# Kernel tuning notes

Hardware: AMD Instinct MI355X
Metric: run time of the kernel (lower is better)

## Reference

```python
import jax, jax.numpy as jnp
import numpy as np

DIM = 2048
HEADS = 16
DIM_HEAD = 128
FF_INNER = DIM * 4
SCALE_BASE = 512
EPS = 1e-5


def setup_inputs() -> dict:
    key = jax.random.key(0)
    k1, k2, k3, k4 = jax.random.split(key, 4)
    fused_out = HEADS * DIM_HEAD + DIM_HEAD + DIM_HEAD + 2 * FF_INNER  # 18688
    x = jax.random.normal(k1, (2, 2048, DIM), dtype=jnp.float32)
    gamma = jnp.ones((DIM,), dtype=jnp.float32)
    W_fused = jax.random.normal(k2, (DIM, fused_out), dtype=jnp.float32) * 0.02
    W_attn_out = jax.random.normal(k3, (HEADS * DIM_HEAD, DIM), dtype=jnp.float32) * 0.02
    W_ff_out = jax.random.normal(k4, (FF_INNER, DIM), dtype=jnp.float32) * 0.02
    return {"x": x, "gamma": gamma, "W_fused": W_fused, "W_attn_out": W_attn_out, "W_ff_out": W_ff_out}


def _rotate_half(t):
    t1, t2 = jnp.split(t, 2, axis=-1)
    return jnp.concatenate((-t2, t1), axis=-1)


def _rotary(n, dtype):
    # RotaryEmbedding with use_xpos=True, scale_base=512
    half = DIM_HEAD // 2
    inv_freq = 1.0 / (10000.0 ** (jnp.arange(0, DIM_HEAD, 2, dtype=dtype) / DIM_HEAD))
    t = jnp.arange(n, dtype=dtype)
    freqs = jnp.einsum('i,j->ij', t, inv_freq)          # [n, half]
    freqs = jnp.concatenate((freqs, freqs), axis=-1)    # [n, dh]
    scale_vec = (jnp.arange(0, DIM_HEAD, 2, dtype=dtype) + 0.4 * DIM_HEAD) / (1.4 * DIM_HEAD)
    power = (t - n // 2) / SCALE_BASE
    scale = scale_vec[None, :] ** power[:, None]        # [n, half]
    scale = jnp.concatenate((scale, scale), axis=-1)    # [n, dh]
    return freqs, scale


def _apply_rope(pos, t, scale):
    return t * jnp.cos(pos) * scale + _rotate_half(t) * jnp.sin(pos) * scale


def reference(x, gamma, W_fused, W_attn_out, W_ff_out):
    b, n, d = x.shape
    # LayerNorm (beta fixed at zero)
    mu = jnp.mean(x, axis=-1, keepdims=True)
    var = jnp.var(x, axis=-1, keepdims=True)
    xn = (x - mu) * jax.lax.rsqrt(var + EPS) * gamma

    proj = xn @ W_fused
    attn_inner = HEADS * DIM_HEAD
    q = proj[..., :attn_inner]
    k = proj[..., attn_inner:attn_inner + DIM_HEAD]
    v = proj[..., attn_inner + DIM_HEAD:attn_inner + 2 * DIM_HEAD]
    ff = proj[..., attn_inner + 2 * DIM_HEAD:]

    q = q.reshape(b, n, HEADS, DIM_HEAD).transpose(0, 2, 1, 3)  # b h n d

    pos, scale = _rotary(n, x.dtype)
    q = _apply_rope(pos, q, scale)            # broadcasts [n,dh] over b,h
    k = _apply_rope(pos, k, 1.0 / scale)      # k is [b, n, dh]

    # multi-query attention, causal
    sim = jnp.einsum('bhid,bjd->bhij', q, k) * (DIM_HEAD ** -0.5)
    causal_mask = jnp.triu(jnp.ones((n, n), dtype=bool), 1)
    sim = jnp.where(causal_mask, jnp.finfo(sim.dtype).min, sim)
    attn = jax.nn.softmax(sim, axis=-1)
    out = jnp.einsum('bhij,bjd->bhid', attn, v)
    out = out.transpose(0, 2, 1, 3).reshape(b, n, attn_inner)
    attn_out = out @ W_attn_out

    # SwiGLU: chunk -> silu(gate) * x
    ff_x, ff_gate = jnp.split(ff, 2, axis=-1)
    ff_out = (jax.nn.silu(ff_gate) * ff_x) @ W_ff_out

    return attn_out + ff_out
```

## Files before the change

### kernel.cpp

```cpp
#include <hip/hip_runtime.h>

typedef __attribute__((ext_vector_type(8))) short short8;
typedef __attribute__((ext_vector_type(4))) float floatx4;
typedef __attribute__((ext_vector_type(8))) unsigned short ushort8;
typedef __attribute__((ext_vector_type(2))) unsigned int uint2v;

#define FOUT 18688
#define FFI  8192
#define CATW 10240

__device__ __forceinline__ float b2f(unsigned short u){
  union { unsigned int i; float f; } v; v.i = ((unsigned int)u) << 16; return v.f;
}
__device__ __forceinline__ unsigned short f2b(float f){
  union { float f; unsigned int i; } v; v.f = f;
  unsigned int r = v.i + 0x7FFFu + ((v.i >> 16) & 1u);
  return (unsigned short)(r >> 16);
}
__device__ __forceinline__ void gld_lds16(const void* g, void* l){
  __builtin_amdgcn_global_load_lds((const __attribute__((address_space(1))) void*)g,
                                   (__attribute__((address_space(3))) void*)l, 16, 0, 0);
}

__global__ __launch_bounds__(256) void ln_kernel(const float* __restrict__ x,
                                                 const float* __restrict__ gamma,
                                                 unsigned short* __restrict__ xn){
  int row = blockIdx.x;
  const float* xr = x + (size_t)row * 2048;
  int tid = threadIdx.x;
  float v[8]; float s = 0.f, s2 = 0.f;
#pragma unroll
  for(int i=0;i<8;i++){ float t = xr[tid + i*256]; v[i]=t; s+=t; s2+=t*t; }
#pragma unroll
  for(int off=32; off>=1; off>>=1){ s += __shfl_down(s, off, 64); s2 += __shfl_down(s2, off, 64); }
  __shared__ float red[8];
  int wv = tid>>6, ln_ = tid&63;
  if(ln_==0){ red[wv] = s; red[wv+4] = s2; }
  __syncthreads();
  s  = red[0]+red[1]+red[2]+red[3];
  s2 = red[4]+red[5]+red[6]+red[7];
  float mu  = s * (1.f/2048.f);
  float var = s2 * (1.f/2048.f) - mu*mu;
  float rstd = rsqrtf(var + 1e-5f);
#pragma unroll
  for(int i=0;i<8;i++){
    float o = (v[i]-mu)*rstd*gamma[tid + i*256];
    xn[(size_t)row*2048 + tid + i*256] = f2b(o);
  }
}

__global__ void tcast_kernel(const float* __restrict__ W, unsigned short* __restrict__ Wt,
                             int R, int C, int S, int O){
  __shared__ float t[32][33];
  int bx = blockIdx.x*32, by = blockIdx.y*32;
  int tx = threadIdx.x, ty = threadIdx.y;
#pragma unroll
  for(int i=0;i<4;i++) t[ty+i*8][tx] = W[(size_t)(by+ty+i*8)*C + bx+tx];
  __syncthreads();
#pragma unroll
  for(int i=0;i<4;i++) Wt[(size_t)(bx+ty+i*8)*S + O + by+tx] = f2b(t[tx][ty+i*8]);
}

__global__ void vtrans_kernel(const unsigned short* __restrict__ proj, unsigned short* __restrict__ vt){
  __shared__ unsigned short t[32][33];
  int b = blockIdx.z;
  int n0 = blockIdx.x*32, d0 = blockIdx.y*32;
  int tx = threadIdx.x, ty = threadIdx.y;
#pragma unroll
  for(int i=0;i<4;i++) t[ty+i*8][tx] = proj[(size_t)(b*2048 + n0+ty+i*8)*FOUT + 2176 + d0+tx];
  __syncthreads();
#pragma unroll
  for(int i=0;i<4;i++) vt[((size_t)b*128 + d0+ty+i*8)*2048 + n0+tx] = t[tx][ty+i*8];
}

__global__ __launch_bounds__(256) void rope_tab_kernel(floatx4* __restrict__ tab){
  int idx = blockIdx.x*256 + threadIdx.x;
  int i = idx >> 6, j = idx & 63;
  float fj = (float)j, fi = (float)i;
  float p = fi * powf(10000.f, -fj*(1.f/64.f));
  float c = cosf(p), s = sinf(p);
  float sv = (2.f*fj + 51.2f) * (1.f/179.2f);
  float pw = (fi - 1024.f) * (1.f/512.f);
  float sc = powf(sv, pw);
  const float att = 0.08838834764831843f;
  floatx4 o; o[0]=c*sc*att; o[1]=s*sc*att; o[2]=c/sc; o[3]=s/sc;
  tab[idx] = o;
}

__global__ __launch_bounds__(256) void rope_kernel(unsigned short* __restrict__ proj,
                                                   const floatx4* __restrict__ tab){
  int row = blockIdx.x;
  int i = row & 2047;
  unsigned short* pr = proj + (size_t)row*FOUT;
  for(int item = threadIdx.x; item < 17*64; item += 256){
    int slot = item >> 6;
    int j = item & 63;
    floatx4 t = tab[i*64 + j];
    float cs = (slot==16) ? t[2] : t[0];
    float ss = (slot==16) ? t[3] : t[1];
    int colbase = (slot<16) ? slot*128 : 2048;
    float x1 = b2f(pr[colbase+j]);
    float x2 = b2f(pr[colbase+j+64]);
    pr[colbase+j]    = f2b(x1*cs - x2*ss);
    pr[colbase+j+64] = f2b(x2*cs + x1*ss);
  }
}

#define SCHED0() __builtin_amdgcn_sched_barrier(0)
#define BARR()   do{ SCHED0(); __builtin_amdgcn_s_barrier(); SCHED0(); }while(0)

template<int MODE>
__global__ __launch_bounds__(512, 2) void gemm8p_kernel(const unsigned short* __restrict__ A,
                                                        const unsigned short* __restrict__ Bt,
                                                        unsigned short* __restrict__ Cb,
                                                        float* __restrict__ Cf,
                                                        int N, int K, int NT, int ntn,
                                                        size_t zstride){
  __shared__ unsigned short lds[65536];
  const int tid = threadIdx.x;
  const int wave = tid>>6, lane = tid&63;
  const int l15 = lane&15, l4 = lane>>4;
  const int wr = wave>>2, wc = wave&3;
  int id = blockIdx.x;
  int cpx = (int)gridDim.x >> 3;
  int swz = (id & 7)*cpx + (id >> 3);
  int tm = swz / ntn, tn = swz - tm*ntn;
  int kbase = (int)blockIdx.z * (NT*64);
  const unsigned short* Ab = A  + (size_t)tm*256*K + kbase;
  const unsigned short* Bb = Bt + (size_t)tn*256*K + kbase;
  if(MODE==1) Cf += (size_t)blockIdx.z * zstride;

  const int r0 = tid>>3;
  const int colc = ((tid&7) ^ (r0&7))*8;
  const int dstw = wave*512;

#define STAGE(t_, h_, isB_) do{ \
    const unsigned short* g_ = (isB_) ? Bb : Ab; \
    int db_ = (((t_)&1)<<15) + ((isB_)<<14) + ((h_)<<13) + dstw; \
    gld_lds16(g_ + (size_t)((h_)*128 + r0)*K + (t_)*64 + colc, &lds[db_]); \
    gld_lds16(g_ + (size_t)((h_)*128 + r0 + 64)*K + (t_)*64 + colc, &lds[db_ + 4096]); \
  }while(0)

  const int sw8 = l15&7;
  const int fo0 = ((l4    )^sw8)*8;
  const int fo1 = ((l4 + 4)^sw8)*8;
  const int albase = (wr*128 + l15)*64;
  const int blbase = 16384 + (wc*64 + l15)*64;

#define RD_A0(buf_, mf_, kk_) a0_[(mf_)*2+(kk_)] = *(const short8*)&lds[(buf_) + albase + (mf_)*1024 + ((kk_)?fo1:fo0)]
#define RD_A1(buf_, mf_, kk_) a1_[(mf_)*2+(kk_)] = *(const short8*)&lds[(buf_) + albase + 4096 + (mf_)*1024 + ((kk_)?fo1:fo0)]
#define RD_B(buf_, nf_, kk_)  b_[(nf_)*2+(kk_)]  = *(const short8*)&lds[(buf_) + blbase + (nf_)*1024 + ((kk_)?fo1:fo0)]
#define MFMA_Q(aarr_, mo_, no_) do{ \
  _Pragma("unroll") for(int kk=0; kk<2; kk++) \
  _Pragma("unroll") for(int mf=0; mf<4; mf++) \
  _Pragma("unroll") for(int nf=0; nf<2; nf++) \
    acc[(mo_)*4+mf][(no_)*2+nf] = __builtin_amdgcn_mfma_f32_16x16x32_bf16( \
      b_[((no_)*2+nf)*2+kk], aarr_[mf*2+kk], acc[(mo_)*4+mf][(no_)*2+nf], 0,0,0); \
}while(0)

  floatx4 acc[8][4];
#pragma unroll
  for(int i=0;i<8;i++)
#pragma unroll
    for(int j=0;j<4;j++) acc[i][j] = (floatx4)0.f;

  short8 a0_[8], a1_[8], b_[8];

  STAGE(0,0,0); STAGE(0,1,0); STAGE(0,0,1); STAGE(0,1,1);
  STAGE(1,0,1); STAGE(1,1,1); STAGE(1,0,0);
  asm volatile("s_waitcnt vmcnt(6)" ::: "memory");
  SCHED0();
  BARR();
#pragma unroll
  for(int mf=0; mf<4; mf++){ RD_A0(0,mf,0); RD_A0(0,mf,1); }
#pragma unroll
  for(int nf=0; nf<2; nf++){ RD_B(0,nf,0); RD_B(0,nf,1); }
  SCHED0();

  for(int t=0; t<NT; ++t){
    const int bufo = (t&1)<<15;
    const int nbuf = bufo ^ 32768;
    if(t+1 < NT) STAGE(t+1,1,0);
    BARR();
    RD_B(bufo,2,0); RD_B(bufo,2,1); RD_B(bufo,3,0); RD_B(bufo,3,1);
    asm volatile("s_waitcnt lgkmcnt(4)" ::: "memory");
    SCHED0();
    __builtin_amdgcn_s_setprio(1);
    MFMA_Q(a0_,0,0);
    __builtin_amdgcn_s_setprio(0);
    BARR();
    if(t+2 < NT) STAGE(t+2,0,1);
    BARR();
#pragma unroll
    for(int mf=0; mf<4; mf++){ RD_A1(bufo,mf,0); RD_A1(bufo,mf,1); }
    asm volatile("s_waitcnt lgkmcnt(8)" ::: "memory");
    SCHED0();
    __builtin_amdgcn_s_setprio(1);
    MFMA_Q(a0_,0,1);
    __builtin_amdgcn_s_setprio(0);
    BARR();
    if(t+2 < NT){
      STAGE(t+2,1,1);
      asm volatile("s_waitcnt vmcnt(8)" ::: "memory");
    } else if(t+1 < NT){
      asm volatile("s_waitcnt vmcnt(4)" ::: "memory");
    }
    SCHED0();
    BARR();
    asm volatile("s_waitcnt lgkmcnt(0)" ::: "memory");
    SCHED0();
    __builtin_amdgcn_s_setprio(1);
    MFMA_Q(a1_,1,0);
    __builtin_amdgcn_s_setprio(0);
    SCHED0();
    if(t+1 < NT){ RD_B(nbuf,0,0); RD_B(nbuf,0,1); RD_B(nbuf,1,0); RD_B(nbuf,1,1); }
    BARR();
    if(t+2 < NT){
      STAGE(t+2,0,0);
      asm volatile("s_waitcnt vmcnt(6)" ::: "memory");
    } else if(t+1 < NT){
      asm volatile("s_waitcnt vmcnt(0)" ::: "memory");
    }
    SCHED0();
    BARR();
    if(t+1 < NT){
#pragma unroll
      for(int mf=0; mf<4; mf++){ RD_A0(nbuf,mf,0); RD_A0(nbuf,mf,1); }
    }
    SCHED0();
    __builtin_amdgcn_s_setprio(1);
    MFMA_Q(a1_,1,1);
    __builtin_amdgcn_s_setprio(0);
    BARR();
  }

  const size_t crow0 = (size_t)tm*256 + wr*128 + l15;
  const size_t ccol0 = (size_t)tn*256 + wc*64 + l4*4;
#pragma unroll
  for(int mi=0; mi<8; mi++){
    size_t row = crow0 + (mi>>2)*64 + (mi&3)*16;
#pragma unroll
    for(int nj=0; nj<4; nj++){
      size_t col = ccol0 + nj*16;
      floatx4 v = acc[mi][nj];
      if(MODE==0){
        uint2v u;
        u[0] = (unsigned int)f2b(v[0]) | ((unsigned int)f2b(v[1])<<16);
        u[1] = (unsigned int)f2b(v[2]) | ((unsigned int)f2b(v[3])<<16);
        *(uint2v*)&Cb[row*N + col] = u;
      } else {
        *(floatx4*)&Cf[row*N + col] = v;
      }
    }
  }
}

__global__ __launch_bounds__(256) void add2_kernel(const float* __restrict__ p0,
                                                   const float* __restrict__ p1,
                                                   float* __restrict__ o, int n4){
  for(int i = blockIdx.x*256 + threadIdx.x; i < n4; i += gridDim.x*256){
    floatx4 a = ((const floatx4*)p0)[i];
    floatx4 b = ((const floatx4*)p1)[i];
    ((floatx4*)o)[i] = a + b;
  }
}

__global__ __launch_bounds__(256) void attn_kernel(const unsigned short* __restrict__ proj,
                                                   const unsigned short* __restrict__ vt,
                                                   unsigned short* __restrict__ ao){
  __shared__ unsigned short lK[64*128];
  __shared__ unsigned short lV[128*64];
  __shared__ unsigned short lP[4*16*64];
  int qt = blockIdx.x, hh = blockIdx.y, b = blockIdx.z;
  int tid = threadIdx.x, wave = tid>>6, lane = tid&63;
  int l15 = lane&15, l4 = lane>>4;
  int q0 = qt*64;
  int qrow = q0 + wave*16 + l15;
  const unsigned short* qp = proj + (size_t)(b*2048 + qrow)*FOUT + hh*128 + l4*8;
  short8 qf[4];
#pragma unroll
  for(int ds=0; ds<4; ds++) qf[ds] = *(const short8*)(qp + ds*32);
  floatx4 po[8];
#pragma unroll
  for(int dt=0; dt<8; dt++) po[dt] = (floatx4)0.f;
  float mrun[4] = {-1e30f,-1e30f,-1e30f,-1e30f};
  float lrun[4] = {0.f,0.f,0.f,0.f};
  unsigned short* lPw = lP + wave*1024;
  const unsigned short* kb = proj + (size_t)(b*2048)*FOUT + 2048;
  const unsigned short* vb = vt + (size_t)b*128*2048;

  for(int kv=0; kv<=qt; kv++){
    int kv0 = kv*64;
#pragma unroll
    for(int it=0; it<4; it++){
      int f = it*256 + tid;
      int r = f>>4, pc = f&15;
      int gc = pc ^ (r&7);
      gld_lds16(kb + (size_t)(kv0 + r)*FOUT + gc*8, &lK[(it*256 + wave*64)*8]);
    }
#pragma unroll
    for(int it=0; it<4; it++){
      int f = it*256 + tid;
      int d = f>>3, pc = f&7;
      int gc = pc ^ (d&7);
      gld_lds16(vb + (size_t)d*2048 + kv0 + gc*8, &lV[(it*256 + wave*64)*8]);
    }
    __syncthreads();
    floatx4 sa[4];
#pragma unroll
    for(int jt=0;jt<4;jt++) sa[jt] = (floatx4)0.f;
#pragma unroll
    for(int jt=0;jt<4;jt++){
      int krow = jt*16 + l15;
#pragma unroll
      for(int ds=0; ds<4; ds++){
        int pc = (l4 + ds*4) ^ (krow&7);
        short8 kf = *(const short8*)&lK[krow*128 + pc*8];
        sa[jt] = __builtin_amdgcn_mfma_f32_16x16x32_bf16(qf[ds], kf, sa[jt], 0,0,0);
      }
    }
    float pv[4][4];
    bool diag = (kv == qt);
#pragma unroll
    for(int jt=0;jt<4;jt++){
#pragma unroll
      for(int r=0;r<4;r++){
        float s = sa[jt][r];
        if(diag && (kv0 + jt*16 + l15 > q0 + wave*16 + l4*4 + r)) s = -1e30f;
        pv[jt][r] = s;
      }
    }
    float mnew[4], corr[4];
#pragma unroll
    for(int r=0;r<4;r++){
      float mx = fmaxf(fmaxf(pv[0][r],pv[1][r]),fmaxf(pv[2][r],pv[3][r]));
      mx = fmaxf(mx, __shfl_xor(mx, 1, 64));
      mx = fmaxf(mx, __shfl_xor(mx, 2, 64));
      mx = fmaxf(mx, __shfl_xor(mx, 4, 64));
      mx = fmaxf(mx, __shfl_xor(mx, 8, 64));
      float mn = fmaxf(mrun[r], mx);
      corr[r] = __expf(mrun[r] - mn);
      mrun[r] = mn;
      mnew[r] = mn;
    }
    float rsum[4] = {0.f,0.f,0.f,0.f};
#pragma unroll
    for(int jt=0;jt<4;jt++){
#pragma unroll
      for(int r=0;r<4;r++){
        float p = __expf(pv[jt][r] - mnew[r]);
        pv[jt][r] = p;
        rsum[r] += p;
      }
    }
#pragma unroll
    for(int r=0;r<4;r++){
      float rs = rsum[r];
      rs += __shfl_xor(rs, 1, 64);
      rs += __shfl_xor(rs, 2, 64);
      rs += __shfl_xor(rs, 4, 64);
      rs += __shfl_xor(rs, 8, 64);
      lrun[r] = lrun[r]*corr[r] + rs;
    }
#pragma unroll
    for(int dt=0;dt<8;dt++){
#pragma unroll
      for(int r=0;r<4;r++) po[dt][r] *= corr[r];
    }
#pragma unroll
    for(int jt=0;jt<4;jt++){
#pragma unroll
      for(int r=0;r<4;r++){
        int i_ = l4*4 + r;
        int j = jt*16 + l15;
        int pc = (j>>3) ^ (i_&7);
        lPw[i_*64 + pc*8 + (j&7)] = f2b(pv[jt][r]);
      }
    }
    asm volatile("s_waitcnt lgkmcnt(0)" ::: "memory");
    short8 pf[2];
#pragma unroll
    for(int ks=0;ks<2;ks++){
      int pc = (l4 + ks*4) ^ (l15&7);
      pf[ks] = *(const short8*)&lPw[l15*64 + pc*8];
    }
#pragma unroll
    for(int dt=0;dt<8;dt++){
      int d = dt*16 + l15;
#pragma unroll
      for(int ks=0;ks<2;ks++){
        int pc = (ks*4 + l4) ^ (d&7);
        short8 vf = *(const short8*)&lV[d*64 + pc*8];
        po[dt] = __builtin_amdgcn_mfma_f32_16x16x32_bf16(pf[ks], vf, po[dt], 0,0,0);
      }
    }
    __syncthreads();
  }
#pragma unroll
  for(int r=0;r<4;r++){
    float inv = 1.f / lrun[r];
    size_t orow = (size_t)(b*2048 + q0 + wave*16 + l4*4 + r);
#pragma unroll
    for(int dt=0;dt<8;dt++){
      ao[orow*CATW + hh*128 + dt*16 + l15] = f2b(po[dt][r]*inv);
    }
  }
}

__global__ __launch_bounds__(256) void swiglu_kernel(const unsigned short* __restrict__ proj,
                                                     unsigned short* __restrict__ cat){
  size_t idx = (size_t)blockIdx.x*256 + threadIdx.x;
  int row = (int)(idx >> 10);
  int c8  = (int)(idx & 1023);
  const unsigned short* pr = proj + (size_t)row*FOUT + 2304 + c8*8;
  ushort8 xv = *(const ushort8*)pr;
  ushort8 gv = *(const ushort8*)(pr + FFI);
  ushort8 ov;
#pragma unroll
  for(int e=0;e<8;e++){
    float xf = b2f(xv[e]);
    float gf = b2f(gv[e]);
    float sg = gf / (1.f + __expf(-gf));
    ov[e] = f2b(sg*xf);
  }
  *(ushort8*)(cat + (size_t)row*CATW + 2048 + c8*8) = ov;
}

extern "C" void kernel_launch(void* const* d_in, const int* in_sizes, int n_in,
                              void* d_out, int out_size, void* d_ws, size_t ws_size,
                              hipStream_t stream){
  const float* x     = (const float*)d_in[0];
  const float* gamma = (const float*)d_in[1];
  const float* Wf    = (const float*)d_in[2];
  const float* Wa    = (const float*)d_in[3];
  const float* Wff   = (const float*)d_in[4];
  float* out = (float*)d_out;

  char* p = (char*)d_ws;
  unsigned short* xn    = (unsigned short*)p;  p += (size_t)4096*2048*2;
  unsigned short* WfT   = (unsigned short*)p;  p += (size_t)18688*2048*2;
  unsigned short* proj  = (unsigned short*)p;  p += (size_t)4096*18688*2;
  unsigned short* BtCat = (unsigned short*)p;  p += (size_t)2048*CATW*2;
  unsigned short* cat   = (unsigned short*)p;  p += (size_t)4096*CATW*2;
  unsigned short* vtb   = (unsigned short*)p;  p += (size_t)2*128*2048*2;
  floatx4*        rtab  = (floatx4*)p;         p += (size_t)2048*64*16;
  float* part = (float*)d_ws;

  ln_kernel<<<4096, 256, 0, stream>>>(x, gamma, xn);
  rope_tab_kernel<<<512, 256, 0, stream>>>(rtab);
  tcast_kernel<<<dim3(584,64),  dim3(32,8), 0, stream>>>(Wf,  WfT,   2048, 18688, 2048, 0);
  tcast_kernel<<<dim3(64,64),   dim3(32,8), 0, stream>>>(Wa,  BtCat, 2048, 2048,  CATW, 0);
  tcast_kernel<<<dim3(64,256),  dim3(32,8), 0, stream>>>(Wff, BtCat, 8192, 2048,  CATW, 2048);
  gemm8p_kernel<0><<<dim3(1168,1,1), 512, 0, stream>>>(xn, WfT, proj, nullptr, 18688, 2048, 32, 73, 0);
  rope_kernel<<<4096, 256, 0, stream>>>(proj, rtab);
  vtrans_kernel<<<dim3(64,4,2), dim3(32,8), 0, stream>>>(proj, vtb);
  attn_kernel<<<dim3(32,16,2), 256, 0, stream>>>(proj, vtb, cat);
  swiglu_kernel<<<16384, 256, 0, stream>>>(proj, cat);
  gemm8p_kernel<1><<<dim3(128,1,2), 512, 0, stream>>>(cat, BtCat, nullptr, part, 2048, 10240, 80, 8,
                                                      (size_t)4096*2048);
  add2_kernel<<<2048, 256, 0, stream>>>(part, part + (size_t)4096*2048, out, 2097152);
}
```

Measured before the change: 861.1 us.

## Simplify GEMM pipeline, change tile mapping, and enlarge attention query tiles

The GEMM main loop drops cross-iteration register prefetch of A/B fragments: each iteration now reads its fragments from LDS at the start. Tile indexing becomes fixed bit ops instead of a division, the MFMA operand order is swapped, and the epilogue writes one element at a time instead of packed vectors. The attention kernel moves to 128-query tiles with 512 threads and launches the heaviest causal blocks first, aiming for better load balance and more reuse of K/V. In exchange, the GEMM gives up overlap between LDS reads and MFMA work and issues narrower global stores.

```diff
diff --git a/kernel.cpp b/kernel.cpp
--- a/kernel.cpp
+++ b/kernel.cpp
@@ -21,6 +21,9 @@
   __builtin_amdgcn_global_load_lds((const __attribute__((address_space(1))) void*)g,
                                    (__attribute__((address_space(3))) void*)l, 16, 0, 0);
 }
+
+#define SCHED0() __builtin_amdgcn_sched_barrier(0)
+#define BARR()   do{ SCHED0(); __builtin_amdgcn_s_barrier(); SCHED0(); }while(0)
 
 __global__ __launch_bounds__(256) void ln_kernel(const float* __restrict__ x,
                                                  const float* __restrict__ gamma,
@@ -106,16 +109,12 @@
   }
 }
 
-#define SCHED0() __builtin_amdgcn_sched_barrier(0)
-#define BARR()   do{ SCHED0(); __builtin_amdgcn_s_barrier(); SCHED0(); }while(0)
-
 template<int MODE>
 __global__ __launch_bounds__(512, 2) void gemm8p_kernel(const unsigned short* __restrict__ A,
                                                         const unsigned short* __restrict__ Bt,
                                                         unsigned short* __restrict__ Cb,
                                                         float* __restrict__ Cf,
-                                                        int N, int K, int NT, int ntn,
-                                                        size_t zstride){
+                                                        int N, int K, int NT, size_t zstride){
   __shared__ unsigned short lds[65536];
   const int tid = threadIdx.x;
   const int wave = tid>>6, lane = tid&63;
@@ -124,7 +123,7 @@
   int id = blockIdx.x;
   int cpx = (int)gridDim.x >> 3;
   int swz = (id & 7)*cpx + (id >> 3);
-  int tm = swz / ntn, tn = swz - tm*ntn;
+  int tm = swz & 15, tn = swz >> 4;
   int kbase = (int)blockIdx.z * (NT*64);
   const unsigned short* Ab = A  + (size_t)tm*256*K + kbase;
   const unsigned short* Bb = Bt + (size_t)tn*256*K + kbase;
@@ -147,15 +146,14 @@
   const int albase = (wr*128 + l15)*64;
   const int blbase = 16384 + (wc*64 + l15)*64;
 
-#define RD_A0(buf_, mf_, kk_) a0_[(mf_)*2+(kk_)] = *(const short8*)&lds[(buf_) + albase + (mf_)*1024 + ((kk_)?fo1:fo0)]
-#define RD_A1(buf_, mf_, kk_) a1_[(mf_)*2+(kk_)] = *(const short8*)&lds[(buf_) + albase + 4096 + (mf_)*1024 + ((kk_)?fo1:fo0)]
-#define RD_B(buf_, nf_, kk_)  b_[(nf_)*2+(kk_)]  = *(const short8*)&lds[(buf_) + blbase + (nf_)*1024 + ((kk_)?fo1:fo0)]
-#define MFMA_Q(aarr_, mo_, no_) do{ \
-  _Pragma("unroll") for(int kk=0; kk<2; kk++) \
+#define RD_A(buf_, mh_, mf_, kk_) a_[(mf_)*2+(kk_)] = *(const short8*)&lds[(buf_) + albase + (mh_)*4096 + (mf_)*1024 + ((kk_)?fo1:fo0)]
+#define RD_B(buf_, nf_, kk_)      b_[(nf_)*2+(kk_)]  = *(const short8*)&lds[(buf_) + blbase + (nf_)*1024 + ((kk_)?fo1:fo0)]
+#define MFMA_Q(mo_, no_) do{ \
   _Pragma("unroll") for(int mf=0; mf<4; mf++) \
   _Pragma("unroll") for(int nf=0; nf<2; nf++) \
+  _Pragma("unroll") for(int kk=0; kk<2; kk++) \
     acc[(mo_)*4+mf][(no_)*2+nf] = __builtin_amdgcn_mfma_f32_16x16x32_bf16( \
-      b_[((no_)*2+nf)*2+kk], aarr_[mf*2+kk], acc[(mo_)*4+mf][(no_)*2+nf], 0,0,0); \
+      a_[mf*2+kk], b_[((no_)*2+nf)*2+kk], acc[(mo_)*4+mf][(no_)*2+nf], 0,0,0); \
 }while(0)
 
   floatx4 acc[8][4];
@@ -163,57 +161,42 @@
   for(int i=0;i<8;i++)
 #pragma unroll
     for(int j=0;j<4;j++) acc[i][j] = (floatx4)0.f;
-
-  short8 a0_[8], a1_[8], b_[8];
 
   STAGE(0,0,0); STAGE(0,1,0); STAGE(0,0,1); STAGE(0,1,1);
   STAGE(1,0,1); STAGE(1,1,1); STAGE(1,0,0);
   asm volatile("s_waitcnt vmcnt(6)" ::: "memory");
-  SCHED0();
   BARR();
-#pragma unroll
-  for(int mf=0; mf<4; mf++){ RD_A0(0,mf,0); RD_A0(0,mf,1); }
-#pragma unroll
-  for(int nf=0; nf<2; nf++){ RD_B(0,nf,0); RD_B(0,nf,1); }
-  SCHED0();
-
+
+  short8 a_[8], b_[8];
   for(int t=0; t<NT; ++t){
     const int bufo = (t&1)<<15;
-    const int nbuf = bufo ^ 32768;
+#pragma unroll
+    for(int mf=0; mf<4; mf++){ RD_A(bufo,0,mf,0); RD_A(bufo,0,mf,1); }
+#pragma unroll
+    for(int nf=0; nf<4; nf++){ RD_B(bufo,nf,0); RD_B(bufo,nf,1); }
     if(t+1 < NT) STAGE(t+1,1,0);
-    BARR();
-    RD_B(bufo,2,0); RD_B(bufo,2,1); RD_B(bufo,3,0); RD_B(bufo,3,1);
-    asm volatile("s_waitcnt lgkmcnt(4)" ::: "memory");
-    SCHED0();
-    __builtin_amdgcn_s_setprio(1);
-    MFMA_Q(a0_,0,0);
-    __builtin_amdgcn_s_setprio(0);
-    BARR();
-    if(t+2 < NT) STAGE(t+2,0,1);
-    BARR();
-#pragma unroll
-    for(int mf=0; mf<4; mf++){ RD_A1(bufo,mf,0); RD_A1(bufo,mf,1); }
-    asm volatile("s_waitcnt lgkmcnt(8)" ::: "memory");
-    SCHED0();
-    __builtin_amdgcn_s_setprio(1);
-    MFMA_Q(a0_,0,1);
-    __builtin_amdgcn_s_setprio(0);
-    BARR();
-    if(t+2 < NT){
-      STAGE(t+2,1,1);
-      asm volatile("s_waitcnt vmcnt(8)" ::: "memory");
-    } else if(t+1 < NT){
-      asm volatile("s_waitcnt vmcnt(4)" ::: "memory");
-    }
-    SCHED0();
     BARR();
     asm volatile("s_waitcnt lgkmcnt(0)" ::: "memory");
     SCHED0();
     __builtin_amdgcn_s_setprio(1);
-    MFMA_Q(a1_,1,0);
+    MFMA_Q(0,0);
     __builtin_amdgcn_s_setprio(0);
+    BARR();
+    if(t+2 < NT) STAGE(t+2,0,1);
+    BARR();
+    __builtin_amdgcn_s_setprio(1);
+    MFMA_Q(0,1);
+    __builtin_amdgcn_s_setprio(0);
+    BARR();
+#pragma unroll
+    for(int mf=0; mf<4; mf++){ RD_A(bufo,1,mf,0); RD_A(bufo,1,mf,1); }
+    if(t+2 < NT) STAGE(t+2,1,1);
+    BARR();
+    asm volatile("s_waitcnt lgkmcnt(0)" ::: "memory");
     SCHED0();
-    if(t+1 < NT){ RD_B(nbuf,0,0); RD_B(nbuf,0,1); RD_B(nbuf,1,0); RD_B(nbuf,1,1); }
+    __builtin_amdgcn_s_setprio(1);
+    MFMA_Q(1,0);
+    __builtin_amdgcn_s_setprio(0);
     BARR();
     if(t+2 < NT){
       STAGE(t+2,0,0);
@@ -223,33 +206,24 @@
     }
     SCHED0();
     BARR();
-    if(t+1 < NT){
-#pragma unroll
-      for(int mf=0; mf<4; mf++){ RD_A0(nbuf,mf,0); RD_A0(nbuf,mf,1); }
-    }
+    __builtin_amdgcn_s_setprio(1);
+    MFMA_Q(1,1);
+    __builtin_amdgcn_s_setprio(0);
     SCHED0();
-    __builtin_amdgcn_s_setprio(1);
-    MFMA_Q(a1_,1,1);
-    __builtin_amdgcn_s_setprio(0);
-    BARR();
-  }
-
-  const size_t crow0 = (size_t)tm*256 + wr*128 + l15;
-  const size_t ccol0 = (size_t)tn*256 + wc*64 + l4*4;
-#pragma unroll
-  for(int mi=0; mi<8; mi++){
-    size_t row = crow0 + (mi>>2)*64 + (mi&3)*16;
-#pragma unroll
-    for(int nj=0; nj<4; nj++){
-      size_t col = ccol0 + nj*16;
-      floatx4 v = acc[mi][nj];
-      if(MODE==0){
-        uint2v u;
-        u[0] = (unsigned int)f2b(v[0]) | ((unsigned int)f2b(v[1])<<16);
-        u[1] = (unsigned int)f2b(v[2]) | ((unsigned int)f2b(v[3])<<16);
-        *(uint2v*)&Cb[row*N + col] = u;
-      } else {
-        *(floatx4*)&Cf[row*N + col] = v;
+    BARR();
+  }
+
+#pragma unroll
+  for(int m=0;m<8;m++){
+#pragma unroll
+    for(int n=0;n<4;n++){
+#pragma unroll
+      for(int r=0;r<4;r++){
+        size_t row = (size_t)tm*256 + wr*128 + (m>>2)*64 + (m&3)*16 + l4*4 + r;
+        size_t col = (size_t)tn*256 + wc*64 + n*16 + l15;
+        float v = acc[m][n][r];
+        if(MODE==0)      Cb[row*N + col] = f2b(v);
+        else             Cf[row*N + col] = v;
       }
     }
   }
@@ -265,16 +239,17 @@
   }
 }
 
-__global__ __launch_bounds__(256) void attn_kernel(const unsigned short* __restrict__ proj,
+__global__ __launch_bounds__(512) void attn_kernel(const unsigned short* __restrict__ proj,
                                                    const unsigned short* __restrict__ vt,
                                                    unsigned short* __restrict__ ao){
   __shared__ unsigned short lK[64*128];
   __shared__ unsigned short lV[128*64];
-  __shared__ unsigned short lP[4*16*64];
-  int qt = blockIdx.x, hh = blockIdx.y, b = blockIdx.z;
+  __shared__ unsigned short lP[8*16*64];
+  int qt = (int)gridDim.x - 1 - (int)blockIdx.x;
+  int hh = blockIdx.y, b = blockIdx.z;
   int tid = threadIdx.x, wave = tid>>6, lane = tid&63;
   int l15 = lane&15, l4 = lane>>4;
-  int q0 = qt*64;
+  int q0 = qt*128;
   int qrow = q0 + wave*16 + l15;
   const unsigned short* qp = proj + (size_t)(b*2048 + qrow)*FOUT + hh*128 + l4*8;
   short8 qf[4];
@@ -288,22 +263,23 @@
   unsigned short* lPw = lP + wave*1024;
   const unsigned short* kb = proj + (size_t)(b*2048)*FOUT + 2048;
   const unsigned short* vb = vt + (size_t)b*128*2048;
-
-  for(int kv=0; kv<=qt; kv++){
+  int kvmax = 2*qt + 1;
+
+  for(int kv=0; kv<=kvmax; kv++){
     int kv0 = kv*64;
 #pragma unroll
-    for(int it=0; it<4; it++){
-      int f = it*256 + tid;
+    for(int it=0; it<2; it++){
+      int f = it*512 + tid;
       int r = f>>4, pc = f&15;
       int gc = pc ^ (r&7);
-      gld_lds16(kb + (size_t)(kv0 + r)*FOUT + gc*8, &lK[(it*256 + wave*64)*8]);
-    }
-#pragma unroll
-    for(int it=0; it<4; it++){
-      int f = it*256 + tid;
+      gld_lds16(kb + (size_t)(kv0 + r)*FOUT + gc*8, &lK[(it*512 + wave*64)*8]);
+    }
+#pragma unroll
+    for(int it=0; it<2; it++){
+      int f = it*512 + tid;
       int d = f>>3, pc = f&7;
       int gc = pc ^ (d&7);
-      gld_lds16(vb + (size_t)d*2048 + kv0 + gc*8, &lV[(it*256 + wave*64)*8]);
+      gld_lds16(vb + (size_t)d*2048 + kv0 + gc*8, &lV[(it*512 + wave*64)*8]);
     }
     __syncthreads();
     floatx4 sa[4];
@@ -320,7 +296,7 @@
       }
     }
     float pv[4][4];
-    bool diag = (kv == qt);
+    bool diag = (kv0 + 63 > q0 + wave*16);
 #pragma unroll
     for(int jt=0;jt<4;jt++){
 #pragma unroll
@@ -451,12 +427,12 @@
   tcast_kernel<<<dim3(584,64),  dim3(32,8), 0, stream>>>(Wf,  WfT,   2048, 18688, 2048, 0);
   tcast_kernel<<<dim3(64,64),   dim3(32,8), 0, stream>>>(Wa,  BtCat, 2048, 2048,  CATW, 0);
   tcast_kernel<<<dim3(64,256),  dim3(32,8), 0, stream>>>(Wff, BtCat, 8192, 2048,  CATW, 2048);
-  gemm8p_kernel<0><<<dim3(1168,1,1), 512, 0, stream>>>(xn, WfT, proj, nullptr, 18688, 2048, 32, 73, 0);
+  gemm8p_kernel<0><<<dim3(1168,1,1), 512, 0, stream>>>(xn, WfT, proj, nullptr, 18688, 2048, 32, 0);
   rope_kernel<<<4096, 256, 0, stream>>>(proj, rtab);
   vtrans_kernel<<<dim3(64,4,2), dim3(32,8), 0, stream>>>(proj, vtb);
-  attn_kernel<<<dim3(32,16,2), 256, 0, stream>>>(proj, vtb, cat);
+  attn_kernel<<<dim3(16,16,2), 512, 0, stream>>>(proj, vtb, cat);
   swiglu_kernel<<<16384, 256, 0, stream>>>(proj, cat);
-  gemm8p_kernel<1><<<dim3(128,1,2), 512, 0, stream>>>(cat, BtCat, nullptr, part, 2048, 10240, 80, 8,
+  gemm8p_kernel<1><<<dim3(128,1,2), 512, 0, stream>>>(cat, BtCat, nullptr, part, 2048, 10240, 80,
                                                       (size_t)4096*2048);
   add2_kernel<<<2048, 256, 0, stream>>>(part, part + (size_t)4096*2048, out, 2097152);
 }
```

Result: faster. 769.9 us (-10.6%).
